# Optimization experiments

Measured on AMD Instinct MI355X. Metric: run time of the kernel, lower is better.

## Reference

```python
import jax, jax.numpy as jnp
import numpy as np
from jax import lax


def setup_inputs() -> dict:
    key = jax.random.key(0)
    k1, k2, k3 = jax.random.split(key, 3)
    B, C, H, W = 32, 256, 64, 64
    x = jax.random.normal(k1, (B, C, H, W), dtype=jnp.float32)
    # ECA conv1d: 1 in-ch, 1 out-ch, kernel 5 (derived from C=256), no bias
    conv1d_w = jax.random.normal(k2, (1, 1, 5), dtype=jnp.float32) * 0.3
    # Spatial conv2d: 2 in-ch, 1 out-ch, kernel 7, with bias
    conv2d_w = jax.random.normal(k3, (1, 2, 7, 7), dtype=jnp.float32) * 0.1
    conv2d_b = jnp.zeros((1,), dtype=jnp.float32)
    return {"x": x, "conv1d_w": conv1d_w, "conv2d_w": conv2d_w, "conv2d_b": conv2d_b}


def reference(x, conv1d_w, conv2d_w, conv2d_b):
    # --- ECA channel attention ---
    # global avg pool over H,W -> [B, C]
    y = jnp.mean(x, axis=(2, 3))
    # conv1d across the channel axis (treated as length), 1 feature channel
    y = y[:, None, :]  # [B, 1, C]
    y = lax.conv_general_dilated(
        y, conv1d_w, window_strides=(1,), padding=[(2, 2)],
        dimension_numbers=("NCH", "OIH", "NCH"))
    ch_w = jax.nn.sigmoid(y)[:, 0, :, None, None]  # [B, C, 1, 1]
    eca_out = x * ch_w

    # --- spatial attention ---
    max_pool = jnp.max(x, axis=1, keepdims=True)   # [B,1,H,W]
    avg_pool = jnp.mean(x, axis=1, keepdims=True)  # [B,1,H,W]
    sp_in = jnp.concatenate([max_pool, avg_pool], axis=1)  # [B,2,H,W]
    sp = lax.conv_general_dilated(
        sp_in, conv2d_w, window_strides=(1, 1), padding=[(3, 3), (3, 3)],
        dimension_numbers=("NCHW", "OIHW", "NCHW"))
    sp = jax.nn.sigmoid(sp + conv2d_b[None, :, None, None])  # [B,1,H,W]

    return eca_out + x * sp + x
```

## Files before the change

### kernel.cpp

```cpp
#include <hip/hip_runtime.h>
#include <math.h>

#define BB 32
#define CC 256
#define HH 64
#define WW 64
#define HWSZ (HH * WW)
#define NCHUNK 16

typedef float f32x4 __attribute__((ext_vector_type(4)));

__global__ __launch_bounds__(256) void stats_kernel(
    const float* __restrict__ x, float* __restrict__ chan_part,
    float* __restrict__ pmax0, float* __restrict__ psum0,
    float* __restrict__ pmax1, float* __restrict__ psum1) {
  const int b = blockIdx.x >> 5;
  const int rem = blockIdx.x & 31;
  const int chunk = rem >> 1;
  const int half = rem & 1;
  const int hw0 = chunk << 8;
  const int tid = threadIdx.x;
  const int wave = tid >> 6;
  const int lane = tid & 63;
  const int c_base = (half << 7) + (wave << 5);

  const float4* xp =
      (const float4*)(x + ((size_t)b << 20) + ((size_t)c_base << 12) + hw0) + lane;

  float4 mx = make_float4(-3.4e38f, -3.4e38f, -3.4e38f, -3.4e38f);
  float4 sm = make_float4(0.f, 0.f, 0.f, 0.f);

  for (int g = 0; g < 2; ++g) {
    float s[16];
#pragma unroll
    for (int ci = 0; ci < 16; ++ci) {
      const float4 v = xp[(g * 16 + ci) * (HWSZ / 4)];
      mx.x = fmaxf(mx.x, v.x); mx.y = fmaxf(mx.y, v.y);
      mx.z = fmaxf(mx.z, v.z); mx.w = fmaxf(mx.w, v.w);
      sm.x += v.x; sm.y += v.y; sm.z += v.z; sm.w += v.w;
      s[ci] = (v.x + v.y) + (v.z + v.w);
    }
#pragma unroll
    for (int ci = 0; ci < 16; ++ci) {
      float v = s[ci];
#pragma unroll
      for (int off = 32; off > 0; off >>= 1) v += __shfl_xor(v, off, 64);
      s[ci] = v;
    }
    if (lane == 0) {
      float4* cp = (float4*)(chan_part +
                             ((size_t)(b * NCHUNK + chunk)) * CC + c_base + g * 16);
      cp[0] = make_float4(s[0],  s[1],  s[2],  s[3]);
      cp[1] = make_float4(s[4],  s[5],  s[6],  s[7]);
      cp[2] = make_float4(s[8],  s[9],  s[10], s[11]);
      cp[3] = make_float4(s[12], s[13], s[14], s[15]);
    }
  }

  __shared__ float4 lmax[4][64];
  __shared__ float4 lsum[4][64];
  lmax[wave][lane] = mx;
  lsum[wave][lane] = sm;
  __syncthreads();
  if (tid < 64) {
    const float4 a = lmax[0][tid], b4 = lmax[1][tid];
    const float4 c4 = lmax[2][tid], d4 = lmax[3][tid];
    float4 M;
    M.x = fmaxf(fmaxf(a.x, b4.x), fmaxf(c4.x, d4.x));
    M.y = fmaxf(fmaxf(a.y, b4.y), fmaxf(c4.y, d4.y));
    M.z = fmaxf(fmaxf(a.z, b4.z), fmaxf(c4.z, d4.z));
    M.w = fmaxf(fmaxf(a.w, b4.w), fmaxf(c4.w, d4.w));
    const float4 sa = lsum[0][tid], sb = lsum[1][tid];
    const float4 sc = lsum[2][tid], sd = lsum[3][tid];
    float4 S;
    S.x = (sa.x + sb.x) + (sc.x + sd.x);
    S.y = (sa.y + sb.y) + (sc.y + sd.y);
    S.z = (sa.z + sb.z) + (sc.z + sd.z);
    S.w = (sa.w + sb.w) + (sc.w + sd.w);
    float* pm = half ? pmax1 : pmax0;
    float* ps = half ? psum1 : psum0;
    ((float4*)(pm + ((size_t)b << 12) + hw0))[tid] = M;
    ((float4*)(ps + ((size_t)b << 12) + hw0))[tid] = S;
  }
}

__global__ __launch_bounds__(256) void attn_kernel(
    const float* __restrict__ chan_part, const float* __restrict__ w5,
    float* __restrict__ ch_w,
    const float* __restrict__ pmax0, const float* __restrict__ psum0,
    const float* __restrict__ pmax1, const float* __restrict__ psum1,
    const float* __restrict__ w2, const float* __restrict__ bias,
    float* __restrict__ sp) {
  if (blockIdx.x < BB) {
    __shared__ float m[CC];
    const int b = blockIdx.x;
    const int c = threadIdx.x;
    float s = 0.0f;
#pragma unroll
    for (int k = 0; k < NCHUNK; ++k)
      s += chan_part[(size_t)(b * NCHUNK + k) * CC + c];
    m[c] = s * (1.0f / HWSZ);
    __syncthreads();

    float acc = 0.0f;
#pragma unroll
    for (int k = 0; k < 5; ++k) {
      int cc = c + k - 2;
      float v = (cc >= 0 && cc < CC) ? m[cc] : 0.0f;
      acc = fmaf(v, w5[k], acc);
    }
    ch_w[b * CC + c] = 1.0f / (1.0f + __expf(-acc));
  } else {
    const int sblk = blockIdx.x - BB;
    const int b = sblk >> 4;
    const int chunk = sblk & 15;
    const int r0 = chunk << 2;
    const int tid = threadIdx.x;

    __shared__ float tmax[10][72];
    __shared__ float tsum[10][72];
    for (int idx = tid; idx < 720; idx += 256) {
      const int row = idx / 72;
      const int col = idx - row * 72;
      const int hh = r0 - 3 + row;
      const int wcol = col - 3;
      float vm = 0.0f, vs = 0.0f;
      if (hh >= 0 && hh < HH && wcol >= 0 && wcol < WW) {
        const int off = (b << 12) + (hh << 6) + wcol;
        vm = fmaxf(pmax0[off], pmax1[off]);
        vs = psum0[off] + psum1[off];
      }
      tmax[row][col] = vm;
      tsum[row][col] = vs;
    }
    __syncthreads();

    const int lr = tid >> 6;
    const int w = tid & 63;
    float acc = bias[0];
#pragma unroll
    for (int kh = 0; kh < 7; ++kh) {
#pragma unroll
      for (int kw = 0; kw < 7; ++kw) {
        acc = fmaf(tmax[lr + kh][w + kw], w2[kh * 7 + kw], acc);
        acc = fmaf(tsum[lr + kh][w + kw], w2[49 + kh * 7 + kw] * (1.0f / CC), acc);
      }
    }
    sp[(b << 12) + (chunk << 8) + tid] = 1.0f / (1.0f + __expf(-acc));
  }
}

__global__ __launch_bounds__(256) void combine_kernel(
    const float* __restrict__ x, const float* __restrict__ ch_w,
    const float* __restrict__ sp, float* __restrict__ out) {
  const int blk = blockIdx.x;
  const int b = blk >> 10;
  const int c = (blk >> 2) & 255;
  const int hw0 = (blk & 3) << 10;
  const int t4 = threadIdx.x;

  const float cw = 1.0f + ch_w[b * CC + c];
  const size_t plane = ((size_t)b << 20) + ((size_t)c << 12) + hw0;
  const float4 x4 = ((const float4*)(x + plane))[t4];
  const float4 s4 = ((const float4*)(sp + ((size_t)b << 12) + hw0))[t4];

  f32x4 o;
  o.x = x4.x * (cw + s4.x);
  o.y = x4.y * (cw + s4.y);
  o.z = x4.z * (cw + s4.z);
  o.w = x4.w * (cw + s4.w);
  __builtin_nontemporal_store(o, (f32x4*)(out + plane) + t4);
}

extern "C" void kernel_launch(void* const* d_in, const int* in_sizes, int n_in,
                              void* d_out, int out_size, void* d_ws, size_t ws_size,
                              hipStream_t stream) {
  const float* x    = (const float*)d_in[0];
  const float* w1   = (const float*)d_in[1];
  const float* w2   = (const float*)d_in[2];
  const float* bias = (const float*)d_in[3];
  float* out = (float*)d_out;

  float* ws = (float*)d_ws;
  float* chan_part = ws;
  float* ch_w      = ws + 131072;
  float* pmax0     = ws + 139264;
  float* psum0     = ws + 270336;
  float* pmax1     = ws + 401408;
  float* psum1     = ws + 532480;
  float* sp        = ws + 663552;

  stats_kernel<<<BB * NCHUNK * 2, 256, 0, stream>>>(
      x, chan_part, pmax0, psum0, pmax1, psum1);
  attn_kernel<<<BB + BB * NCHUNK, 256, 0, stream>>>(
      chan_part, w1, ch_w, pmax0, psum0, pmax1, psum1, w2, bias, sp);
  combine_kernel<<<(BB * CC * HWSZ) / (4 * 256), 256, 0, stream>>>(x, ch_w, sp, out);
}
```

Measured before the change: 259.7 us.

## Restructure stats kernel: wider spatial tiles per wave, four channel-quarter partials

The stats kernel now has each block cover a 1024-element spatial quarter and a 64-channel quarter. Each wave handles 16 channels and loads four float4 per channel per iteration. It does one shuffle reduction per channel instead of per-lane partial arrays, and writes four channel-quarter partial max/sum planes instead of two. The attention kernel merges four partials instead of two. The aim is more memory-level parallelism and fewer shuffle reductions per byte loaded, at the cost of doubling the partial-plane traffic read by the spatial conv.

```diff
diff --git a/kernel.cpp b/kernel.cpp
--- a/kernel.cpp
+++ b/kernel.cpp
@@ -6,89 +6,100 @@
 #define HH 64
 #define WW 64
 #define HWSZ (HH * WW)
-#define NCHUNK 16
 
 typedef float f32x4 __attribute__((ext_vector_type(4)));
 
 __global__ __launch_bounds__(256) void stats_kernel(
     const float* __restrict__ x, float* __restrict__ chan_part,
-    float* __restrict__ pmax0, float* __restrict__ psum0,
-    float* __restrict__ pmax1, float* __restrict__ psum1) {
-  const int b = blockIdx.x >> 5;
-  const int rem = blockIdx.x & 31;
-  const int chunk = rem >> 1;
-  const int half = rem & 1;
-  const int hw0 = chunk << 8;
+    float* __restrict__ pmax, float* __restrict__ psum) {
+  const int b = blockIdx.x >> 4;
+  const int q = (blockIdx.x >> 2) & 3;
+  const int cq = blockIdx.x & 3;
   const int tid = threadIdx.x;
   const int wave = tid >> 6;
   const int lane = tid & 63;
-  const int c_base = (half << 7) + (wave << 5);
-
-  const float4* xp =
-      (const float4*)(x + ((size_t)b << 20) + ((size_t)c_base << 12) + hw0) + lane;
-
-  float4 mx = make_float4(-3.4e38f, -3.4e38f, -3.4e38f, -3.4e38f);
-  float4 sm = make_float4(0.f, 0.f, 0.f, 0.f);
-
-  for (int g = 0; g < 2; ++g) {
-    float s[16];
-#pragma unroll
-    for (int ci = 0; ci < 16; ++ci) {
-      const float4 v = xp[(g * 16 + ci) * (HWSZ / 4)];
-      mx.x = fmaxf(mx.x, v.x); mx.y = fmaxf(mx.y, v.y);
-      mx.z = fmaxf(mx.z, v.z); mx.w = fmaxf(mx.w, v.w);
-      sm.x += v.x; sm.y += v.y; sm.z += v.z; sm.w += v.w;
-      s[ci] = (v.x + v.y) + (v.z + v.w);
-    }
-#pragma unroll
-    for (int ci = 0; ci < 16; ++ci) {
-      float v = s[ci];
-#pragma unroll
-      for (int off = 32; off > 0; off >>= 1) v += __shfl_xor(v, off, 64);
-      s[ci] = v;
-    }
-    if (lane == 0) {
-      float4* cp = (float4*)(chan_part +
-                             ((size_t)(b * NCHUNK + chunk)) * CC + c_base + g * 16);
-      cp[0] = make_float4(s[0],  s[1],  s[2],  s[3]);
-      cp[1] = make_float4(s[4],  s[5],  s[6],  s[7]);
-      cp[2] = make_float4(s[8],  s[9],  s[10], s[11]);
-      cp[3] = make_float4(s[12], s[13], s[14], s[15]);
-    }
-  }
-
-  __shared__ float4 lmax[4][64];
-  __shared__ float4 lsum[4][64];
-  lmax[wave][lane] = mx;
-  lsum[wave][lane] = sm;
+  const int c0 = (cq << 6) + (wave << 4);
+
+  __shared__ float4 lmax[4][4][64];
+  __shared__ float4 lsum[4][4][64];
+
+  float4 mx[4], sm[4];
+#pragma unroll
+  for (int g = 0; g < 4; ++g) {
+    mx[g] = make_float4(-3.4e38f, -3.4e38f, -3.4e38f, -3.4e38f);
+    sm[g] = make_float4(0.f, 0.f, 0.f, 0.f);
+  }
+  float own = 0.0f;
+
+  const float4* xb =
+      (const float4*)(x + ((size_t)b << 20) + ((size_t)c0 << 12) + (q << 10)) + lane;
+
+#pragma unroll 2
+  for (int ci = 0; ci < 16; ++ci) {
+    const float4* xc = xb + ci * (HWSZ / 4);
+    const float4 v0 = xc[0];
+    const float4 v1 = xc[64];
+    const float4 v2 = xc[128];
+    const float4 v3 = xc[192];
+
+    mx[0].x = fmaxf(mx[0].x, v0.x); mx[0].y = fmaxf(mx[0].y, v0.y);
+    mx[0].z = fmaxf(mx[0].z, v0.z); mx[0].w = fmaxf(mx[0].w, v0.w);
+    mx[1].x = fmaxf(mx[1].x, v1.x); mx[1].y = fmaxf(mx[1].y, v1.y);
+    mx[1].z = fmaxf(mx[1].z, v1.z); mx[1].w = fmaxf(mx[1].w, v1.w);
+    mx[2].x = fmaxf(mx[2].x, v2.x); mx[2].y = fmaxf(mx[2].y, v2.y);
+    mx[2].z = fmaxf(mx[2].z, v2.z); mx[2].w = fmaxf(mx[2].w, v2.w);
+    mx[3].x = fmaxf(mx[3].x, v3.x); mx[3].y = fmaxf(mx[3].y, v3.y);
+    mx[3].z = fmaxf(mx[3].z, v3.z); mx[3].w = fmaxf(mx[3].w, v3.w);
+
+    sm[0].x += v0.x; sm[0].y += v0.y; sm[0].z += v0.z; sm[0].w += v0.w;
+    sm[1].x += v1.x; sm[1].y += v1.y; sm[1].z += v1.z; sm[1].w += v1.w;
+    sm[2].x += v2.x; sm[2].y += v2.y; sm[2].z += v2.z; sm[2].w += v2.w;
+    sm[3].x += v3.x; sm[3].y += v3.y; sm[3].z += v3.z; sm[3].w += v3.w;
+
+    float s = ((v0.x + v0.y) + (v0.z + v0.w)) + ((v1.x + v1.y) + (v1.z + v1.w)) +
+              ((v2.x + v2.y) + (v2.z + v2.w)) + ((v3.x + v3.y) + (v3.z + v3.w));
+#pragma unroll
+    for (int off = 32; off > 0; off >>= 1) s += __shfl_xor(s, off, 64);
+    if (lane == ci) own = s;
+  }
+
+  if (lane < 16)
+    chan_part[(size_t)((b << 2) + q) * CC + c0 + lane] = own;
+
+#pragma unroll
+  for (int g = 0; g < 4; ++g) {
+    lmax[wave][g][lane] = mx[g];
+    lsum[wave][g][lane] = sm[g];
+  }
   __syncthreads();
-  if (tid < 64) {
-    const float4 a = lmax[0][tid], b4 = lmax[1][tid];
-    const float4 c4 = lmax[2][tid], d4 = lmax[3][tid];
+
+  {
+    const int g = tid >> 6;
+    const int l = tid & 63;
+    const float4 a = lmax[0][g][l], b4 = lmax[1][g][l];
+    const float4 c4 = lmax[2][g][l], d4 = lmax[3][g][l];
     float4 M;
     M.x = fmaxf(fmaxf(a.x, b4.x), fmaxf(c4.x, d4.x));
     M.y = fmaxf(fmaxf(a.y, b4.y), fmaxf(c4.y, d4.y));
     M.z = fmaxf(fmaxf(a.z, b4.z), fmaxf(c4.z, d4.z));
     M.w = fmaxf(fmaxf(a.w, b4.w), fmaxf(c4.w, d4.w));
-    const float4 sa = lsum[0][tid], sb = lsum[1][tid];
-    const float4 sc = lsum[2][tid], sd = lsum[3][tid];
+    const float4 sa = lsum[0][g][l], sb = lsum[1][g][l];
+    const float4 sc = lsum[2][g][l], sd = lsum[3][g][l];
     float4 S;
     S.x = (sa.x + sb.x) + (sc.x + sd.x);
     S.y = (sa.y + sb.y) + (sc.y + sd.y);
     S.z = (sa.z + sb.z) + (sc.z + sd.z);
     S.w = (sa.w + sb.w) + (sc.w + sd.w);
-    float* pm = half ? pmax1 : pmax0;
-    float* ps = half ? psum1 : psum0;
-    ((float4*)(pm + ((size_t)b << 12) + hw0))[tid] = M;
-    ((float4*)(ps + ((size_t)b << 12) + hw0))[tid] = S;
+    const int f4 = ((cq * BB + b) << 10) + (q << 8) + (g << 6) + l;
+    ((float4*)pmax)[f4] = M;
+    ((float4*)psum)[f4] = S;
   }
 }
 
 __global__ __launch_bounds__(256) void attn_kernel(
     const float* __restrict__ chan_part, const float* __restrict__ w5,
     float* __restrict__ ch_w,
-    const float* __restrict__ pmax0, const float* __restrict__ psum0,
-    const float* __restrict__ pmax1, const float* __restrict__ psum1,
+    const float* __restrict__ pmax, const float* __restrict__ psum,
     const float* __restrict__ w2, const float* __restrict__ bias,
     float* __restrict__ sp) {
   if (blockIdx.x < BB) {
@@ -97,8 +108,8 @@
     const int c = threadIdx.x;
     float s = 0.0f;
 #pragma unroll
-    for (int k = 0; k < NCHUNK; ++k)
-      s += chan_part[(size_t)(b * NCHUNK + k) * CC + c];
+    for (int k = 0; k < 4; ++k)
+      s += chan_part[(size_t)((b << 2) + k) * CC + c];
     m[c] = s * (1.0f / HWSZ);
     __syncthreads();
 
@@ -127,8 +138,11 @@
       float vm = 0.0f, vs = 0.0f;
       if (hh >= 0 && hh < HH && wcol >= 0 && wcol < WW) {
         const int off = (b << 12) + (hh << 6) + wcol;
-        vm = fmaxf(pmax0[off], pmax1[off]);
-        vs = psum0[off] + psum1[off];
+        const float m0 = pmax[off], m1 = pmax[(BB << 12) + off];
+        const float m2 = pmax[(2 * BB << 12) + off], m3 = pmax[(3 * BB << 12) + off];
+        vm = fmaxf(fmaxf(m0, m1), fmaxf(m2, m3));
+        vs = (psum[off] + psum[(BB << 12) + off]) +
+             (psum[(2 * BB << 12) + off] + psum[(3 * BB << 12) + off]);
       }
       tmax[row][col] = vm;
       tsum[row][col] = vs;
@@ -183,16 +197,13 @@
 
   float* ws = (float*)d_ws;
   float* chan_part = ws;
-  float* ch_w      = ws + 131072;
-  float* pmax0     = ws + 139264;
-  float* psum0     = ws + 270336;
-  float* pmax1     = ws + 401408;
-  float* psum1     = ws + 532480;
-  float* sp        = ws + 663552;
-
-  stats_kernel<<<BB * NCHUNK * 2, 256, 0, stream>>>(
-      x, chan_part, pmax0, psum0, pmax1, psum1);
-  attn_kernel<<<BB + BB * NCHUNK, 256, 0, stream>>>(
-      chan_part, w1, ch_w, pmax0, psum0, pmax1, psum1, w2, bias, sp);
+  float* ch_w      = ws + 32768;
+  float* pmax      = ws + 40960;
+  float* psum      = ws + 565248;
+  float* sp        = ws + 1089536;
+
+  stats_kernel<<<BB * 16, 256, 0, stream>>>(x, chan_part, pmax, psum);
+  attn_kernel<<<BB + BB * 16, 256, 0, stream>>>(
+      chan_part, w1, ch_w, pmax, psum, w2, bias, sp);
   combine_kernel<<<(BB * CC * HWSZ) / (4 * 256), 256, 0, stream>>>(x, ch_w, sp, out);
 }
```

Result: no change. 258.0 us (-0.7%).
